# Kernel optimization log

Hardware: AMD Instinct MI355X
Metric: run time of the kernel (lower is better)

## Reference

```python
import jax, jax.numpy as jnp
import numpy as np


def setup_inputs() -> dict:
    key = jax.random.key(0)
    x = jax.random.normal(key, (8, 2048, 3), dtype=jnp.float32)
    return {"x": x, "k": 16}


def reference(x, k):
    b, n, d = x.shape
    xf = x.reshape(b * n, d)                      # flatten across batch, as in the torch module
    sq = jnp.sum(xf * xf, axis=1, keepdims=True)  # [BN, 1]
    pair = 2.0 * (xf @ xf.T) - sq - sq.T          # [BN, BN] = -dist^2
    # torch topk(largest=False) on pair == largest of (-pair) == largest squared distance
    neg_vals, idx = jax.lax.top_k(-pair, k + 1)   # [BN, k+1]
    dists = -neg_vals
    dists = dists[:, 1:].reshape(b, n, k)
    idx = idx[:, 1:].reshape(b, n, k)
    return dists, idx
```

## Files before the change

kernel.cpp:

```cpp
#include <hip/hip_runtime.h>
#include <stdint.h>

#define BN       16384
#define NTILES   256
#define NB       64
#define KOUT     16
#define MARGIN   0.01f

typedef float v2f __attribute__((ext_vector_type(2)));
union F4 { float4 f4; v2f p[2]; float f[4]; };

#define WS_TAB    0
#define WS_IDX    (WS_TAB + BN * 16)
#define WS_BND    (WS_IDX + BN * 4)
#define WS_HIST   (WS_BND + NTILES * 8)
#define WS_HMAX   (WS_HIST + 64 * NB * 4)

__device__ __forceinline__ unsigned key_u(unsigned u) {
    return u ^ ((unsigned)((int)u >> 31) | 0x80000000u);
}
__device__ __forceinline__ unsigned wshr1(unsigned v, unsigned oldv) {
    return (unsigned)__builtin_amdgcn_update_dpp((int)oldv, (int)v, 0x138 ,
                                                 0xF, 0xF, false);
}
#define RL16(T) __uint_as_float((unsigned)__builtin_amdgcn_readlane(__float_as_int(T), 16))

__device__ __forceinline__ float sq_of(float gx, float gy, float gz) {
    return __fadd_rn(__fadd_rn(__fmul_rn(gx, gx), __fmul_rn(gy, gy)), __fmul_rn(gz, gz));
}
__device__ __forceinline__ int bucket_of(float sq) {
    const float rho = __fsqrt_rn(sq);
    int b = (int)(64.0f * (1.0f - rho * 0.2f));
    return (b < 0) ? 0 : ((b > 63) ? 63 : b);
}

#define DRAIN(m, p, jvec, T, J)                                                     \
    while (m) {                                                                     \
        const int b_ = (int)__builtin_ctzll(m);                                     \
        m &= m - 1;                                                                 \
        const float pc_ = __uint_as_float(                                          \
            (unsigned)__builtin_amdgcn_readlane(__float_as_int(p), b_));            \
        const unsigned jc_ = (unsigned)__builtin_amdgcn_readlane((int)(jvec), b_);  \
        const float Tup_ =                                                          \
            __uint_as_float(wshr1(__float_as_uint(T), 0xFF800000u ));       \
        const unsigned Jup_ = wshr1((J), 0u);                                       \
        const bool lt_ = (pc_ < Tup_) || ((pc_ == Tup_) && (jc_ < Jup_));           \
        const float Tn_ = lt_ ? Tup_ : pc_;                                         \
        const unsigned Jn_ = lt_ ? Jup_ : jc_;                                      \
        const bool sel_ = (pc_ < (T)) || ((pc_ == (T)) && (jc_ < (J)));             \
        (T) = sel_ ? Tn_ : (T);                                                     \
        (J) = sel_ ? Jn_ : (J);                                                     \
    }

#define EVALC(c, d2)                                                                \
    asm("v_pk_mul_f32 %0, %1, %2 op_sel:[0,0] op_sel_hi:[0,1]"                      \
        : "=v"(d2) : "v"((c).p[0]), "v"(c0A));                                      \
    asm("v_pk_fma_f32 %0, %1, %2, %0 op_sel:[1,0,0] op_sel_hi:[1,1,1]"              \
        : "+v"(d2) : "v"((c).p[0]), "v"(c1A));                                      \
    asm("v_pk_fma_f32 %0, %1, %2, %0 op_sel:[0,0,0] op_sel_hi:[0,1,1]"              \
        : "+v"(d2) : "v"((c).p[1]), "v"(c2A));                                      \
    asm("v_pk_add_f32 %0, %0, %1" : "+v"(d2) : "v"(nsq01));                         \
    asm("v_pk_add_f32 %0, %0, %1 op_sel:[0,1] op_sel_hi:[1,1]"                      \
        : "+v"(d2) : "v"((c).p[1]));

#define CERTM(bd)                                                                    \
    __ballot((__builtin_fmaf(twor0, (bd)[1], __fadd_rn(sq0, (bd)[0])) < thr0) &&     \
             (__builtin_fmaf(twor1, (bd)[1], __fadd_rn(sq1, (bd)[0])) < thr1))

#define COMPUTE_TSTAR()                                                              \
    do {                                                                             \
        uint64_t mm;                                                                 \
        if ((mm = CERTM(bdA)))        ts = (int)__builtin_ctzll(mm);                 \
        else if ((mm = CERTM(bdB)))   ts = 64  + (int)__builtin_ctzll(mm);           \
        else if ((mm = CERTM(bdC)))   ts = 128 + (int)__builtin_ctzll(mm);           \
        else if ((mm = CERTM(bdD)))   ts = 192 + (int)__builtin_ctzll(mm);           \
        else                          ts = NTILES;                                   \
    } while (0)

#define PROC1(c, t)                                                                  \
    {                                                                                \
        v2f d2; EVALC(c, d2)                                                         \
        uint64_t m0 = __ballot(d2[0] <= fF0);                                        \
        uint64_t m1 = __ballot(d2[1] <= fF1);                                        \
        if (m0 | m1) {                                                               \
            const unsigned jvec = (unsigned)idx16[(t) * 64 + lane];                  \
            const float p0v = d2[0], p1v = d2[1];                                    \
            DRAIN(m0, p0v, jvec, T0, J0)                                             \
            DRAIN(m1, p1v, jvec, T1, J1)                                             \
            fF0 = RL16(T0); thr0 = __fsub_rn(-fF0, MARGIN);                          \
            fF1 = RL16(T1); thr1 = __fsub_rn(-fF1, MARGIN);                          \
            COMPUTE_TSTAR();                                                         \
        }                                                                            \
    }

__device__ __forceinline__ void presort2(float p0, float p1, unsigned j, int lane,
                                         uint4* sw,
                                         float& T0c, unsigned& J0c,
                                         float& T1c, unsigned& J1c) {
    const unsigned kp0 = key_u(__float_as_uint(p0));
    const unsigned kp1 = key_u(__float_as_uint(p1));
    const unsigned long long k0 = ((unsigned long long)kp0 << 32) | (unsigned long long)j;
    const unsigned long long k1 = ((unsigned long long)kp1 << 32) | (unsigned long long)j;
    sw[lane] = make_uint4(j, kp0, j, kp1);
    unsigned r0 = 0u, r1 = 0u;
    unsigned off = (unsigned)lane;
#pragma unroll 7
    for (int s = 1; s < 64; ++s) {
        off = (off + 1u) & 63u;
        const uint4 o = sw[off];
        const unsigned long long o0 = ((unsigned long long)o.y << 32) | (unsigned long long)o.x;
        const unsigned long long o1 = ((unsigned long long)o.w << 32) | (unsigned long long)o.z;
        r0 += (o0 < k0) ? 1u : 0u;
        r1 += (o1 < k1) ? 1u : 0u;
    }
    unsigned long long* s0 = (unsigned long long*)sw;
    unsigned long long* s1 = s0 + 64;
    s0[r0] = k0;
    s1[r1] = k1;
    const unsigned long long v0 = s0[lane];
    const unsigned long long v1 = s1[lane];
    const unsigned kq0 = (unsigned)(v0 >> 32), kq1 = (unsigned)(v1 >> 32);
    T0c = __uint_as_float((kq0 & 0x80000000u) ? (kq0 ^ 0x80000000u) : ~kq0);
    J0c = (unsigned)(v0 & 0xFFFFFFFFull);
    T1c = __uint_as_float((kq1 & 0x80000000u) ? (kq1 ^ 0x80000000u) : ~kq1);
    J1c = (unsigned)(v1 & 0xFFFFFFFFull);
}

__global__ __launch_bounds__(256) void k_hist(const float* __restrict__ x,
                                              unsigned* __restrict__ hist,
                                              unsigned* __restrict__ hmax) {
    __shared__ unsigned h[NB], m[NB];
    const int tid = threadIdx.x;
    if (tid < NB) { h[tid] = 0u; m[tid] = 0u; }
    __syncthreads();
    const int i = blockIdx.x * 256 + tid;
    const float sq = sq_of(x[3 * i], x[3 * i + 1], x[3 * i + 2]);
    const int b = bucket_of(sq);
    atomicAdd(&h[b], 1u);
    atomicMax(&m[b], __float_as_uint(sq));
    __syncthreads();
    if (tid < NB) {
        hist[blockIdx.x * NB + tid] = h[tid];
        hmax[blockIdx.x * NB + tid] = m[tid];
    }
}

__global__ __launch_bounds__(256) void k_prep(const float* __restrict__ x,
                                              const unsigned* __restrict__ hist,
                                              const unsigned* __restrict__ hmax,
                                              float4* __restrict__ tab,
                                              unsigned short* __restrict__ idx16,
                                              float2* __restrict__ bnd) {
    __shared__ unsigned colbase[NB], cur[NB], basev[NB + 1], mxv[NB], sfxs[NB];
    const int tid = threadIdx.x;
    const int blk = blockIdx.x;
    if (tid < NB) {
        unsigned tot = 0u, part = 0u, mx = 0u;
#pragma unroll 8
        for (int g = 0; g < 64; ++g) {
            const unsigned h = hist[g * NB + tid];
            tot += h;
            part += (g < blk) ? h : 0u;
            const unsigned w = hmax[g * NB + tid];
            mx = (w > mx) ? w : mx;
        }
        unsigned v = tot;
#pragma unroll
        for (int s = 1; s < 64; s <<= 1) {
            const unsigned n = (unsigned)__shfl_up((int)v, (unsigned)s, 64);
            v += (tid >= s) ? n : 0u;
        }
        basev[tid] = v - tot;
        if (tid == NB - 1) basev[NB] = v;
        colbase[tid] = (v - tot) + part;
        cur[tid] = 0u;
        mxv[tid] = mx;
    }
    __syncthreads();
    const int i = blk * 256 + tid;
    const float gx = x[3 * i], gy = x[3 * i + 1], gz = x[3 * i + 2];
    const float sq = sq_of(gx, gy, gz);
    const int b = bucket_of(sq);
    const unsigned r = atomicAdd(&cur[b], 1u);
    const unsigned pos = colbase[b] + r;
    tab[pos] = make_float4(gx, gy, gz, -sq);
    idx16[pos] = (unsigned short)i;

    if (blk == 0) {
        if (tid == 0) {
            unsigned M = 0u;
            for (int b2 = NB - 1; b2 >= 0; --b2) {
                const unsigned w = mxv[b2];
                M = (w > M) ? w : M;
                sfxs[b2] = M;
            }
        }
        __syncthreads();
        const unsigned posb = (unsigned)tid * 64u;
        int bb = 0;
        for (int t2 = 0; t2 < NB; ++t2)
            if (basev[t2] <= posb && posb < basev[t2 + 1]) bb = t2;
        const float B = __uint_as_float(sfxs[bb]);
        const float sqB_up = __uint_as_float(__float_as_uint(__fsqrt_rn(B)) + 2u);
        bnd[tid] = make_float2(B, sqB_up);
    }
}

__global__ __launch_bounds__(256) void knn_far_kernel(
    const float4* __restrict__ tab, const unsigned short* __restrict__ idx16,
    const float2* __restrict__ bnd, float* __restrict__ out_d, float* __restrict__ out_i) {
    __shared__ uint4 swall[4][64];
    const int tid  = threadIdx.x;
    const int lane = tid & 63;
    const int wid  = tid >> 6;
    uint4* sw = swall[wid];
    const int p0 = (blockIdx.x * 4 + wid) * 2;
    const int p1 = p0 + 1;

    F4 qa; qa.f4 = tab[p0];
    F4 qb; qb.f4 = tab[p1];
    const unsigned q0 = (unsigned)idx16[p0];
    const unsigned q1 = (unsigned)idx16[p1];
    const float sq0 = -qa.f[3], sq1 = -qb.f[3];
    const v2f nsq01 = {qa.f[3], qb.f[3]};
    const v2f c0A = {2.0f * qa.f[0], 2.0f * qb.f[0]};
    const v2f c1A = {2.0f * qa.f[1], 2.0f * qb.f[1]};
    const v2f c2A = {2.0f * qa.f[2], 2.0f * qb.f[2]};
    const float twor0 = 2.0f * __uint_as_float(__float_as_uint(__fsqrt_rn(sq0)) + 2u);
    const float twor1 = 2.0f * __uint_as_float(__float_as_uint(__fsqrt_rn(sq1)) + 2u);

    const v2f* bndv = (const v2f*)bnd;
    const v2f bdA = bndv[lane];
    const v2f bdB = bndv[64 + lane];
    const v2f bdC = bndv[128 + lane];
    const v2f bdD = bndv[192 + lane];

    float T0, T1; unsigned J0, J1;
    float fF0, fF1, thr0, thr1;
    int ts = NTILES;

    {
        F4 s0_, s1_, s2_, s3_;
        s0_.f4 = tab[0 * 64 + lane];
        s1_.f4 = tab[1 * 64 + lane];
        s2_.f4 = tab[2 * 64 + lane];
        s3_.f4 = tab[3 * 64 + lane];
        const unsigned jv0 = (unsigned)idx16[lane];
        {
            v2f d2; EVALC(s0_, d2)
            presort2(d2[0], d2[1], jv0, lane, sw, T0, J0, T1, J1);
            fF0 = RL16(T0); thr0 = __fsub_rn(-fF0, MARGIN);
            fF1 = RL16(T1); thr1 = __fsub_rn(-fF1, MARGIN);
        }
        PROC1(s1_, 1)
        PROC1(s2_, 2)
        PROC1(s3_, 3)
    }

    COMPUTE_TSTAR();

    for (int t = 4; t < ts; t += 4) {
        F4 cA_, cB_, cC_, cD_;
        cA_.f4 = tab[(t + 0) * 64 + lane];
        cB_.f4 = tab[(t + 1) * 64 + lane];
        cC_.f4 = tab[(t + 2) * 64 + lane];
        cD_.f4 = tab[(t + 3) * 64 + lane];
        PROC1(cA_, t + 0)
        PROC1(cB_, t + 1)
        PROC1(cC_, t + 2)
        PROC1(cD_, t + 3)
    }

    if (lane >= 1 && lane <= KOUT) {
        const int r = lane - 1;
        out_d[q0 * KOUT + r] = T0;
        out_i[q0 * KOUT + r] = (float)J0;
        out_d[q1 * KOUT + r] = T1;
        out_i[q1 * KOUT + r] = (float)J1;
    }
}

extern "C" void kernel_launch(void* const* d_in, const int* in_sizes, int n_in,
                              void* d_out, int out_size, void* d_ws, size_t ws_size,
                              hipStream_t stream) {
    const float* x = (const float*)d_in[0];
    char* ws = (char*)d_ws;
    float4*         tab   = (float4*)(ws + WS_TAB);
    unsigned short* idx16 = (unsigned short*)(ws + WS_IDX);
    float2*         bnd   = (float2*)(ws + WS_BND);
    unsigned*       hist  = (unsigned*)(ws + WS_HIST);
    unsigned*       hmax  = (unsigned*)(ws + WS_HMAX);
    float* out_d = (float*)d_out;
    float* out_i = out_d + (size_t)BN * KOUT;

    hipLaunchKernelGGL(k_hist, dim3(64), dim3(256), 0, stream, x, hist, hmax);
    hipLaunchKernelGGL(k_prep, dim3(64), dim3(256), 0, stream, x, hist, hmax,
                       tab, idx16, bnd);
    hipLaunchKernelGGL(knn_far_kernel, dim3(BN / 8), dim3(256), 0, stream,
                       tab, idx16, bnd, out_d, out_i);
}
```

Before: 77.40 us.

## Fuse histogram and prep kernels using an in-kernel grid barrier

Merges the histogram kernel and the prep/scatter kernel into one 64-block launch. A software grid barrier built on per-block magic flags in workspace synchronises them: each block publishes its histogram, sets its flag, then spins until all flags are set. The goal is to remove one kernel launch and its dependency gap, and to avoid reloading x. The flag values are identical on every call and are never reset, so on repeated calls the barrier can pass immediately and read stale or partial histograms, which is a correctness race. It also relies on all 64 blocks being co-resident.

```diff
diff --git a/kernel.cpp b/kernel.cpp
--- a/kernel.cpp
+++ b/kernel.cpp
@@ -7,13 +7,17 @@
 #define KOUT     16
 #define MARGIN   0.01f
 
+#define MAGIC1   0x5AFEC0DEu
+#define MAGIC2   0xC001D00Du
+
 typedef float v2f __attribute__((ext_vector_type(2)));
 union F4 { float4 f4; v2f p[2]; float f[4]; };
 
 #define WS_TAB    0
 #define WS_IDX    (WS_TAB + BN * 16)
 #define WS_BND    (WS_IDX + BN * 4)
-#define WS_HIST   (WS_BND + NTILES * 8)
+#define WS_FLG    0x60000
+#define WS_HIST   0x70000
 #define WS_HMAX   (WS_HIST + 64 * NB * 4)
 
 __device__ __forceinline__ unsigned key_u(unsigned u) {
@@ -126,41 +130,59 @@
     J1c = (unsigned)(v1 & 0xFFFFFFFFull);
 }
 
-__global__ __launch_bounds__(256) void k_hist(const float* __restrict__ x,
-                                              unsigned* __restrict__ hist,
-                                              unsigned* __restrict__ hmax) {
+__global__ __launch_bounds__(256) void k_prep_f2(const float* __restrict__ x,
+                                                 unsigned* __restrict__ hist,
+                                                 unsigned* __restrict__ hmax,
+                                                 unsigned long long* __restrict__ flg,
+                                                 float4* __restrict__ tab,
+                                                 unsigned short* __restrict__ idx16,
+                                                 float2* __restrict__ bnd) {
     __shared__ unsigned h[NB], m[NB];
+    __shared__ unsigned colbase[NB], cur[NB], basev[NB + 1], mxv[NB], sfxs[NB];
     const int tid = threadIdx.x;
+    const int blk = blockIdx.x;
     if (tid < NB) { h[tid] = 0u; m[tid] = 0u; }
     __syncthreads();
-    const int i = blockIdx.x * 256 + tid;
-    const float sq = sq_of(x[3 * i], x[3 * i + 1], x[3 * i + 2]);
+
+    const int i = blk * 256 + tid;
+    const float gx = x[3 * i], gy = x[3 * i + 1], gz = x[3 * i + 2];
+    const float sq = sq_of(gx, gy, gz);
     const int b = bucket_of(sq);
     atomicAdd(&h[b], 1u);
     atomicMax(&m[b], __float_as_uint(sq));
     __syncthreads();
     if (tid < NB) {
-        hist[blockIdx.x * NB + tid] = h[tid];
-        hmax[blockIdx.x * NB + tid] = m[tid];
-    }
-}
-
-__global__ __launch_bounds__(256) void k_prep(const float* __restrict__ x,
-                                              const unsigned* __restrict__ hist,
-                                              const unsigned* __restrict__ hmax,
-                                              float4* __restrict__ tab,
-                                              unsigned short* __restrict__ idx16,
-                                              float2* __restrict__ bnd) {
-    __shared__ unsigned colbase[NB], cur[NB], basev[NB + 1], mxv[NB], sfxs[NB];
-    const int tid = threadIdx.x;
-    const int blk = blockIdx.x;
+        __hip_atomic_store(&hist[blk * NB + tid], h[tid],
+                           __ATOMIC_RELAXED, __HIP_MEMORY_SCOPE_AGENT);
+        __hip_atomic_store(&hmax[blk * NB + tid], m[tid],
+                           __ATOMIC_RELAXED, __HIP_MEMORY_SCOPE_AGENT);
+    }
+    __syncthreads();
+    if (tid == 0) {
+        const unsigned long long fv =
+            ((unsigned long long)(MAGIC2 ^ (unsigned)blk) << 32) |
+            (unsigned long long)(MAGIC1 + (unsigned)blk);
+        __hip_atomic_store(&flg[blk], fv, __ATOMIC_RELEASE, __HIP_MEMORY_SCOPE_AGENT);
+        for (int t = 0; t < NB; ++t) {
+            const unsigned long long want =
+                ((unsigned long long)(MAGIC2 ^ (unsigned)t) << 32) |
+                (unsigned long long)(MAGIC1 + (unsigned)t);
+            while (__hip_atomic_load(&flg[t], __ATOMIC_RELAXED,
+                                     __HIP_MEMORY_SCOPE_AGENT) != want) {
+                __builtin_amdgcn_s_sleep(16);
+            }
+        }
+        __threadfence();
+    }
+    __syncthreads();
+
     if (tid < NB) {
         unsigned tot = 0u, part = 0u, mx = 0u;
 #pragma unroll 8
         for (int g = 0; g < 64; ++g) {
-            const unsigned h = hist[g * NB + tid];
-            tot += h;
-            part += (g < blk) ? h : 0u;
+            const unsigned hh = hist[g * NB + tid];
+            tot += hh;
+            part += (g < blk) ? hh : 0u;
             const unsigned w = hmax[g * NB + tid];
             mx = (w > mx) ? w : mx;
         }
@@ -177,10 +199,6 @@
         mxv[tid] = mx;
     }
     __syncthreads();
-    const int i = blk * 256 + tid;
-    const float gx = x[3 * i], gy = x[3 * i + 1], gz = x[3 * i + 2];
-    const float sq = sq_of(gx, gy, gz);
-    const int b = bucket_of(sq);
     const unsigned r = atomicAdd(&cur[b], 1u);
     const unsigned pos = colbase[b] + r;
     tab[pos] = make_float4(gx, gy, gz, -sq);
@@ -285,17 +303,17 @@
                               hipStream_t stream) {
     const float* x = (const float*)d_in[0];
     char* ws = (char*)d_ws;
-    float4*         tab   = (float4*)(ws + WS_TAB);
-    unsigned short* idx16 = (unsigned short*)(ws + WS_IDX);
-    float2*         bnd   = (float2*)(ws + WS_BND);
-    unsigned*       hist  = (unsigned*)(ws + WS_HIST);
-    unsigned*       hmax  = (unsigned*)(ws + WS_HMAX);
+    float4*             tab   = (float4*)(ws + WS_TAB);
+    unsigned short*     idx16 = (unsigned short*)(ws + WS_IDX);
+    float2*             bnd   = (float2*)(ws + WS_BND);
+    unsigned long long* flg   = (unsigned long long*)(ws + WS_FLG);
+    unsigned*           hist  = (unsigned*)(ws + WS_HIST);
+    unsigned*           hmax  = (unsigned*)(ws + WS_HMAX);
     float* out_d = (float*)d_out;
     float* out_i = out_d + (size_t)BN * KOUT;
 
-    hipLaunchKernelGGL(k_hist, dim3(64), dim3(256), 0, stream, x, hist, hmax);
-    hipLaunchKernelGGL(k_prep, dim3(64), dim3(256), 0, stream, x, hist, hmax,
-                       tab, idx16, bnd);
+    hipLaunchKernelGGL(k_prep_f2, dim3(64), dim3(256), 0, stream,
+                       x, hist, hmax, flg, tab, idx16, bnd);
     hipLaunchKernelGGL(knn_far_kernel, dim3(BN / 8), dim3(256), 0, stream,
                        tab, idx16, bnd, out_d, out_i);
 }
```

New measurement: 86.52 us. 1.12x slower.
